# Kernel optimization log

Hardware: AMD Instinct MI355X
Metric: run time of the kernel (lower is better)

Reference implementation:

```python
import jax, jax.numpy as jnp
import numpy as np

B, S, D, H, E, K, F = 8, 2048, 1024, 16, 32, 8, 1024
HD = D // H
EPS = 1e-5


def _ln(x, scale, bias):
    m = jnp.mean(x, axis=-1, keepdims=True)
    v = jnp.mean(jnp.square(x - m), axis=-1, keepdims=True)
    return (x - m) * jax.lax.rsqrt(v + EPS) * scale + bias


def setup_inputs() -> dict:
    key = jax.random.key(0)
    ks = jax.random.split(key, 14)
    w = lambda k, shp: jax.random.normal(k, shp, jnp.float32) * 0.02
    return {
        "hidden_states": jax.random.normal(ks[0], (B, S, D), jnp.float32),
        "ln1_scale": jnp.ones((D,), jnp.float32),
        "ln1_bias": jnp.zeros((D,), jnp.float32),
        "wq": w(ks[1], (D, D)), "bq": jnp.zeros((D,), jnp.float32),
        "wk": w(ks[2], (D, D)), "bk": jnp.zeros((D,), jnp.float32),
        "wv": w(ks[3], (D, D)), "bv": jnp.zeros((D,), jnp.float32),
        "ln2_scale": jnp.ones((D,), jnp.float32),
        "ln2_bias": jnp.zeros((D,), jnp.float32),
        "router_w": w(ks[4], (D, E)), "router_b": jnp.zeros((E,), jnp.float32),
        "w1": w(ks[5], (E, D, F)), "b1": jnp.zeros((E, F), jnp.float32),
        "w2": w(ks[6], (E, F, D)), "b2": jnp.zeros((E, D), jnp.float32),
    }


def reference(hidden_states, ln1_scale, ln1_bias, wq, bq, wk, bk, wv, bv,
              ln2_scale, ln2_bias, router_w, router_b, w1, b1, w2, b2):
    # --- attention sub-block (faithful to source: scores are [B,S,H,H]) ---
    x = _ln(hidden_states, ln1_scale, ln1_bias)
    q = (x @ wq + bq).reshape(B, S, H, HD)
    k = (x @ wk + bk).reshape(B, S, H, HD)
    v = (x @ wv + bv).reshape(B, S, H, HD)
    scores = jnp.einsum('bshd,bsgd->bshg', q, k) / np.sqrt(HD).astype(np.float32)
    probs = jax.nn.softmax(scores, axis=-1)
    ctx = jnp.einsum('bshg,bsgd->bshd', probs, v).reshape(B, S, D)
    h1 = hidden_states + ctx
    # --- MoE sub-block: per-token top-K of E experts ---
    x2 = _ln(h1, ln2_scale, ln2_bias)
    router_probs = jax.nn.softmax(x2 @ router_w + router_b, axis=-1)  # [B,S,E]
    top_w, top_i = jax.lax.top_k(router_probs, K)
    top_w = top_w / jnp.sum(top_w, axis=-1, keepdims=True)
    # dense per-token gate over experts (zero for unselected)
    gates = jnp.sum(jax.nn.one_hot(top_i, E, dtype=x2.dtype) * top_w[..., None], axis=-2)  # [B,S,E]
    moe = jnp.zeros_like(x2)
    for e in range(E):  # fixed small expert set; unrolled under jit
        h = jax.nn.gelu(x2 @ w1[e] + b1[e], approximate=False)
        moe = moe + gates[..., e:e + 1] * (h @ w2[e] + b2[e])
    return h1 + moe
```

## Files before the change

kernel.cpp:

```cpp
#include <hip/hip_runtime.h>
#include <hip/hip_bf16.h>
#include <stdint.h>

#define TOK 16384
#define DD  1024
#define NE  32

typedef unsigned short u16;
typedef __attribute__((ext_vector_type(8))) short short8;
typedef __attribute__((ext_vector_type(4))) float f32x4;

__device__ __forceinline__ u16 f2bf(float f) {
  unsigned int u = __float_as_uint(f);
  u += 0x7fffu + ((u >> 16) & 1u);
  return (u16)(u >> 16);
}
__device__ __forceinline__ float bf2f(u16 h) {
  return __uint_as_float(((unsigned int)h) << 16);
}
__device__ __forceinline__ void gload16(const void* g, void* l) {
  __builtin_amdgcn_global_load_lds((const __attribute__((address_space(1))) void*)g,
                                   (__attribute__((address_space(3))) void*)l, 16, 0, 0);
}

__global__ __launch_bounds__(256) void k_transpose(const float* __restrict__ src,
                                                   u16* __restrict__ dst, int R, int C) {
  __shared__ float tile[32][33];
  size_t mb = (size_t)blockIdx.z * R * C;
  int c0 = blockIdx.x * 32, r0 = blockIdx.y * 32;
  int tx = threadIdx.x, ty = threadIdx.y;
#pragma unroll
  for (int i = 0; i < 4; i++)
    tile[ty + i * 8][tx] = src[mb + (size_t)(r0 + ty + i * 8) * C + c0 + tx];
  __syncthreads();
#pragma unroll
  for (int i = 0; i < 4; i++) {
    float v = tile[tx][ty + i * 8];
    dst[mb + (size_t)(c0 + ty + i * 8) * R + r0 + tx] = f2bf(v);
  }
}

__global__ __launch_bounds__(256) void k_transpose_split(const float* __restrict__ src,
                                                         u16* __restrict__ hi,
                                                         u16* __restrict__ lo, int R, int C) {
  __shared__ float tile[32][33];
  int c0 = blockIdx.x * 32, r0 = blockIdx.y * 32;
  int tx = threadIdx.x, ty = threadIdx.y;
#pragma unroll
  for (int i = 0; i < 4; i++)
    tile[ty + i * 8][tx] = src[(size_t)(r0 + ty + i * 8) * C + c0 + tx];
  __syncthreads();
#pragma unroll
  for (int i = 0; i < 4; i++) {
    float v = tile[tx][ty + i * 8];
    u16 h = f2bf(v);
    u16 l = f2bf(v - bf2f(h));
    size_t idx = (size_t)(c0 + ty + i * 8) * R + r0 + tx;
    hi[idx] = h;
    lo[idx] = l;
  }
}

__global__ __launch_bounds__(256) void k_ln1(const float* __restrict__ x,
                                             const float* __restrict__ sc,
                                             const float* __restrict__ bi,
                                             u16* __restrict__ ohi, u16* __restrict__ olo) {
  __shared__ float red[10];
  int t = blockIdx.x, tid = threadIdx.x;
  size_t base = (size_t)t * DD + tid * 4;
  float4 v = *(const float4*)(x + base);
  float s1 = v.x + v.y + v.z + v.w;
  float s2 = v.x * v.x + v.y * v.y + v.z * v.z + v.w * v.w;
  for (int o = 1; o < 64; o <<= 1) { s1 += __shfl_xor(s1, o, 64); s2 += __shfl_xor(s2, o, 64); }
  int wid = tid >> 6;
  if ((tid & 63) == 0) { red[wid * 2] = s1; red[wid * 2 + 1] = s2; }
  __syncthreads();
  if (tid == 0) {
    float a = 0, b = 0;
    for (int i = 0; i < 4; i++) { a += red[i * 2]; b += red[i * 2 + 1]; }
    float mean = a * (1.f / DD);
    float var = b * (1.f / DD) - mean * mean;
    red[8] = mean; red[9] = rsqrtf(var + 1e-5f);
  }
  __syncthreads();
  float mean = red[8], rs = red[9];
  int e0 = tid * 4;
  float xv[4] = {v.x, v.y, v.z, v.w};
  ushort4 oh, ol;
  u16* ph = (u16*)&oh; u16* pl = (u16*)&ol;
#pragma unroll
  for (int i = 0; i < 4; i++) {
    float f = (xv[i] - mean) * rs * sc[e0 + i] + bi[e0 + i];
    u16 h = f2bf(f);
    ph[i] = h;
    pl[i] = f2bf(f - bf2f(h));
  }
  *(ushort4*)(ohi + base) = oh;
  *(ushort4*)(olo + base) = ol;
}

__global__ __launch_bounds__(256) void k_attn(
    const float* __restrict__ hidden, const float* __restrict__ qb,
    const float* __restrict__ kb, const float* __restrict__ vb,
    const float* __restrict__ ln2s, const float* __restrict__ ln2b,
    const float* __restrict__ rw, const float* __restrict__ rb,
    float* __restrict__ out, u16* __restrict__ x2b, float* __restrict__ gates) {
  __shared__ float qs[16][68], ks[16][68], vs[16][68];
  __shared__ float probs[16][17];
  __shared__ float x2s[1024];
  __shared__ float red[12];
  __shared__ float part[8][32];
  int t = blockIdx.x, tid = threadIdx.x;
  size_t base = (size_t)t * DD + tid * 4;
  int hh = tid >> 4, dd = (tid & 15) * 4;
  {
    float4 q4 = *(const float4*)(qb + base);
    float4 k4 = *(const float4*)(kb + base);
    float4 v4 = *(const float4*)(vb + base);
    qs[hh][dd + 0] = q4.x; qs[hh][dd + 1] = q4.y; qs[hh][dd + 2] = q4.z; qs[hh][dd + 3] = q4.w;
    ks[hh][dd + 0] = k4.x; ks[hh][dd + 1] = k4.y; ks[hh][dd + 2] = k4.z; ks[hh][dd + 3] = k4.w;
    vs[hh][dd + 0] = v4.x; vs[hh][dd + 1] = v4.y; vs[hh][dd + 2] = v4.z; vs[hh][dd + 3] = v4.w;
  }
  __syncthreads();
  {
    int g = tid & 15;
    float s = 0.f;
#pragma unroll
    for (int d = 0; d < 64; d++) s += qs[hh][d] * ks[g][d];
    s *= 0.125f;
    float mx = s;
    for (int o = 1; o < 16; o <<= 1) mx = fmaxf(mx, __shfl_xor(mx, o, 16));
    float p = __expf(s - mx);
    float sm = p;
    for (int o = 1; o < 16; o <<= 1) sm += __shfl_xor(sm, o, 16);
    probs[hh][g] = p / sm;
  }
  __syncthreads();
  float c0 = 0, c1 = 0, c2 = 0, c3 = 0;
#pragma unroll
  for (int g = 0; g < 16; g++) {
    float pw = probs[hh][g];
    c0 += pw * vs[g][dd + 0]; c1 += pw * vs[g][dd + 1];
    c2 += pw * vs[g][dd + 2]; c3 += pw * vs[g][dd + 3];
  }
  float4 hv = *(const float4*)(hidden + base);
  float h0 = hv.x + c0, h1 = hv.y + c1, h2 = hv.z + c2, h3 = hv.w + c3;
  { float4 o4; o4.x = h0; o4.y = h1; o4.z = h2; o4.w = h3; *(float4*)(out + base) = o4; }
  float s1 = h0 + h1 + h2 + h3;
  float s2 = h0 * h0 + h1 * h1 + h2 * h2 + h3 * h3;
  for (int o = 1; o < 64; o <<= 1) { s1 += __shfl_xor(s1, o, 64); s2 += __shfl_xor(s2, o, 64); }
  int wid = tid >> 6;
  if ((tid & 63) == 0) { red[wid * 2] = s1; red[wid * 2 + 1] = s2; }
  __syncthreads();
  if (tid == 0) {
    float a = 0, b = 0;
    for (int i = 0; i < 4; i++) { a += red[i * 2]; b += red[i * 2 + 1]; }
    float mean = a * (1.f / DD);
    float var = b * (1.f / DD) - mean * mean;
    red[8] = mean; red[9] = rsqrtf(var + 1e-5f);
  }
  __syncthreads();
  float mean = red[8], rs = red[9];
  int e0 = tid * 4;
  float x0 = (h0 - mean) * rs * ln2s[e0 + 0] + ln2b[e0 + 0];
  float x1 = (h1 - mean) * rs * ln2s[e0 + 1] + ln2b[e0 + 1];
  float x2 = (h2 - mean) * rs * ln2s[e0 + 2] + ln2b[e0 + 2];
  float x3 = (h3 - mean) * rs * ln2s[e0 + 3] + ln2b[e0 + 3];
  ushort4 xo; xo.x = f2bf(x0); xo.y = f2bf(x1); xo.z = f2bf(x2); xo.w = f2bf(x3);
  *(ushort4*)(x2b + base) = xo;
  x2s[e0 + 0] = x0; x2s[e0 + 1] = x1; x2s[e0 + 2] = x2; x2s[e0 + 3] = x3;
  __syncthreads();
  {
    int e = tid & 31, seg = tid >> 5;
    const float* rwp = rw + (size_t)(seg * 128) * NE + e;
    float acc = 0.f;
#pragma unroll 8
    for (int i = 0; i < 128; i++) acc += x2s[seg * 128 + i] * rwp[(size_t)i * NE];
    part[seg][e] = acc;
  }
  __syncthreads();
  if (tid < 32) {
    float l = rb[tid];
#pragma unroll
    for (int s = 0; s < 8; s++) l += part[s][tid];
    float mx = l;
    for (int o = 1; o < 32; o <<= 1) mx = fmaxf(mx, __shfl_xor(mx, o, 32));
    float p = __expf(l - mx);
    float sm = p;
    for (int o = 1; o < 32; o <<= 1) sm += __shfl_xor(sm, o, 32);
    p /= sm;
    bool sel = false;
#pragma unroll
    for (int rsel = 0; rsel < 8; rsel++) {
      float bv = sel ? -1.f : p;
      int bi_ = tid;
      for (int o = 1; o < 32; o <<= 1) {
        float ov = __shfl_xor(bv, o, 32);
        int oi = __shfl_xor(bi_, o, 32);
        if (ov > bv || (ov == bv && oi < bi_)) { bv = ov; bi_ = oi; }
      }
      if (tid == bi_) sel = true;
    }
    float wsel = sel ? p : 0.f;
    float ts = wsel;
    for (int o = 1; o < 32; o <<= 1) ts += __shfl_xor(ts, o, 32);
    gates[(size_t)t * 32 + tid] = sel ? (p / ts) : 0.f;
  }
}

__global__ void k_zero32(int* p) { int i = threadIdx.x; if (i < 32) p[i] = 0; }

__global__ void k_listbuild(const float* __restrict__ gates, int* __restrict__ counts,
                            int* __restrict__ lists, int* __restrict__ slots,
                            float* __restrict__ gsel) {
  int t = blockIdx.x * 256 + threadIdx.x;
  int j = 0;
  for (int e = 0; e < NE; e++) {
    float g = gates[(size_t)t * 32 + e];
    if (g > 0.f && j < 8) {
      int pos = atomicAdd(&counts[e], 1);
      lists[(size_t)e * TOK + pos] = t;
      slots[t * 8 + j] = (e << 14) | pos;
      gsel[t * 8 + j] = g;
      j++;
    }
  }
}

__global__ void k_scan(const int* __restrict__ counts, int* __restrict__ segoff) {
  if (threadIdx.x == 0) { int s = 0; for (int e = 0; e < NE; e++) { segoff[e] = s; s += counts[e]; } }
}

__global__ __launch_bounds__(256) void k_gemm_p(
    const u16* __restrict__ Ahi, const u16* __restrict__ Alo,
    const u16* __restrict__ qkvT,
    const float* __restrict__ bq, const float* __restrict__ bk, const float* __restrict__ bv,
    float* __restrict__ Cbase) {
  constexpr int KD = 1024;
  __shared__ alignas(16) u16 As[2][2][128 * 32];
  __shared__ alignas(16) u16 Bs[2][2][128 * 32];
  const int tid = threadIdx.x;
  const int w = tid >> 6, lane = tid & 63;
  const int bm = blockIdx.x, bn = blockIdx.y, z = blockIdx.z;
  const u16* Bhi = qkvT + (size_t)z * (2u * KD * KD);
  const u16* Blo = Bhi + (size_t)KD * KD;
  const float* bias = (z == 0) ? bq : (z == 1) ? bk : bv;
  float* C = Cbase + (size_t)z * TOK * KD;

  int rowA[2], qA[2], rowB[2];
#pragma unroll
  for (int i = 0; i < 2; i++) {
    int c = (w * 2 + i) * 64 + lane;
    int r = c >> 2;
    qA[i] = c & 3;
    rowB[i] = bn * 128 + r;
    rowA[i] = bm * 128 + r;
  }

  auto stage = [&](int buf, int k0) {
#pragma unroll
    for (int i = 0; i < 2; i++) {
      size_t ga = (size_t)rowA[i] * KD + k0 + qA[i] * 8;
      size_t gb = (size_t)rowB[i] * KD + k0 + qA[i] * 8;
      int lo_off = (w * 2 + i) * 1024;
      gload16(Ahi + ga, (char*)&As[buf][0][0] + lo_off);
      gload16(Alo + ga, (char*)&As[buf][1][0] + lo_off);
      gload16(Bhi + gb, (char*)&Bs[buf][0][0] + lo_off);
      gload16(Blo + gb, (char*)&Bs[buf][1][0] + lo_off);
    }
  };

  f32x4 acc[4][4];
#pragma unroll
  for (int m = 0; m < 4; m++)
#pragma unroll
    for (int n = 0; n < 4; n++) acc[m][n] = (f32x4)0.f;

  const int wr = (w >> 1) * 64, wc = (w & 1) * 64;
  const int la = lane & 15, lk = (lane >> 4) * 8;

  stage(0, 0);
  __syncthreads();
  for (int kt = 0; kt < 32; kt++) {
    const int cur = kt & 1;
    if (kt + 1 < 32) stage(cur ^ 1, (kt + 1) * 32);
    short8 ah[4], al[4], bh[4], bl[4];
#pragma unroll
    for (int m = 0; m < 4; m++) {
      ah[m] = *(const short8*)&As[cur][0][(wr + m * 16 + la) * 32 + lk];
      al[m] = *(const short8*)&As[cur][1][(wr + m * 16 + la) * 32 + lk];
    }
#pragma unroll
    for (int n = 0; n < 4; n++) {
      bh[n] = *(const short8*)&Bs[cur][0][(wc + n * 16 + la) * 32 + lk];
      bl[n] = *(const short8*)&Bs[cur][1][(wc + n * 16 + la) * 32 + lk];
    }
#pragma unroll
    for (int m = 0; m < 4; m++)
#pragma unroll
      for (int n = 0; n < 4; n++) {
        acc[m][n] = __builtin_amdgcn_mfma_f32_16x16x32_bf16(ah[m], bh[n], acc[m][n], 0, 0, 0);
        acc[m][n] = __builtin_amdgcn_mfma_f32_16x16x32_bf16(ah[m], bl[n], acc[m][n], 0, 0, 0);
        acc[m][n] = __builtin_amdgcn_mfma_f32_16x16x32_bf16(al[m], bh[n], acc[m][n], 0, 0, 0);
      }
    __syncthreads();
  }

  const int rl4 = (lane >> 4) * 4;
#pragma unroll
  for (int m = 0; m < 4; m++) {
#pragma unroll
    for (int n = 0; n < 4; n++) {
      const int col = bn * 128 + wc + n * 16 + la;
      const float bvv = bias[col];
      f32x4 a4 = acc[m][n];
#pragma unroll
      for (int r = 0; r < 4; r++) {
        const int grow = bm * 128 + wr + m * 16 + rl4 + r;
        C[(size_t)grow * KD + col] = a4[r] + bvv;
      }
    }
  }
}

__global__ __launch_bounds__(256) void k_gemm1(
    const u16* __restrict__ A, const u16* __restrict__ BT, const float* __restrict__ bias,
    u16* __restrict__ Cb, const int* __restrict__ lists, const int* __restrict__ counts,
    const int* __restrict__ segoff) {
  constexpr int KD = 1024;
  __shared__ alignas(16) u16 As[2][128 * 32];
  __shared__ alignas(16) u16 Bs[2][128 * 32];

  int e = (int)blockIdx.z;
  int count = counts[e];
  if ((int)blockIdx.x * 128 >= count) return;
  const int* list = lists + (size_t)e * TOK;
  int so = segoff[e];
  const u16* Bp = BT + (size_t)e * (KD * KD);
  const float* bp = bias + (size_t)e * KD;

  const int tid = threadIdx.x;
  const int w = tid >> 6, lane = tid & 63;
  const int bm = blockIdx.x, bn = blockIdx.y;

  int rowA[2], qA[2], rowB[2];
#pragma unroll
  for (int i = 0; i < 2; i++) {
    int c = (w * 2 + i) * 64 + lane;
    int r = c >> 2;
    qA[i] = c & 3;
    rowB[i] = bn * 128 + r;
    int rr = bm * 128 + r;
    rowA[i] = (rr < count) ? list[rr] : 0;
  }

  auto stage = [&](int buf, int k0) {
#pragma unroll
    for (int i = 0; i < 2; i++) {
      gload16(A + (size_t)rowA[i] * KD + k0 + qA[i] * 8,
              (char*)&As[buf][0] + (w * 2 + i) * 1024);
      gload16(Bp + (size_t)rowB[i] * KD + k0 + qA[i] * 8,
              (char*)&Bs[buf][0] + (w * 2 + i) * 1024);
    }
  };

  f32x4 acc[4][4];
#pragma unroll
  for (int m = 0; m < 4; m++)
#pragma unroll
    for (int n = 0; n < 4; n++) acc[m][n] = (f32x4)0.f;

  const int wr = (w >> 1) * 64, wc = (w & 1) * 64;
  const int la = lane & 15, lk = (lane >> 4) * 8;

  stage(0, 0);
  __syncthreads();
#pragma unroll 2
  for (int kt = 0; kt < 32; kt++) {
    const int cur = kt & 1;
    if (kt + 1 < 32) stage(cur ^ 1, (kt + 1) * 32);
    short8 af[4], bf8[4];
#pragma unroll
    for (int m = 0; m < 4; m++)
      af[m] = *(const short8*)&As[cur][(wr + m * 16 + la) * 32 + lk];
#pragma unroll
    for (int n = 0; n < 4; n++)
      bf8[n] = *(const short8*)&Bs[cur][(wc + n * 16 + la) * 32 + lk];
#pragma unroll
    for (int m = 0; m < 4; m++)
#pragma unroll
      for (int n = 0; n < 4; n++)
        acc[m][n] = __builtin_amdgcn_mfma_f32_16x16x32_bf16(af[m], bf8[n], acc[m][n], 0, 0, 0);
    __syncthreads();
  }

  const int rl4 = (lane >> 4) * 4;
#pragma unroll
  for (int m = 0; m < 4; m++) {
#pragma unroll
    for (int n = 0; n < 4; n++) {
      const int col = bn * 128 + wc + n * 16 + la;
      const float bvv = bp[col];
      f32x4 a4 = acc[m][n];
#pragma unroll
      for (int r = 0; r < 4; r++) {
        const int grow = bm * 128 + wr + m * 16 + rl4 + r;
        if (grow < count) {
          float v = a4[r] + bvv;
          float gx = 0.5f * v * (1.0f + erff(v * 0.70710678f));
          Cb[(size_t)(so + grow) * KD + col] = f2bf(gx);
        }
      }
    }
  }
}

__global__ __launch_bounds__(256) void k_gemm2(
    const u16* __restrict__ A, const u16* __restrict__ BT, const float* __restrict__ bias,
    u16* __restrict__ out2, const int* __restrict__ counts, const int* __restrict__ segoff,
    int col0, int C) {
  constexpr int KD = 1024;
  __shared__ alignas(16) u16 As[2][128 * 32];
  __shared__ alignas(16) u16 Bs[2][128 * 32];

  int e = (int)blockIdx.z;
  int count = counts[e];
  if ((int)blockIdx.x * 128 >= count) return;
  int so = segoff[e];
  const u16* Bp = BT + (size_t)e * (KD * KD);
  const float* bp = bias + (size_t)e * KD;

  const int tid = threadIdx.x;
  const int w = tid >> 6, lane = tid & 63;
  const int bm = blockIdx.x, bn = blockIdx.y;

  int rowA[2], qA[2], rowB[2];
#pragma unroll
  for (int i = 0; i < 2; i++) {
    int c = (w * 2 + i) * 64 + lane;
    int r = c >> 2;
    qA[i] = c & 3;
    rowB[i] = col0 + bn * 128 + r;
    int rr = bm * 128 + r;
    rowA[i] = so + ((rr < count) ? rr : 0);
  }

  auto stage = [&](int buf, int k0) {
#pragma unroll
    for (int i = 0; i < 2; i++) {
      gload16(A + (size_t)rowA[i] * KD + k0 + qA[i] * 8,
              (char*)&As[buf][0] + (w * 2 + i) * 1024);
      gload16(Bp + (size_t)rowB[i] * KD + k0 + qA[i] * 8,
              (char*)&Bs[buf][0] + (w * 2 + i) * 1024);
    }
  };

  f32x4 acc[4][4];
#pragma unroll
  for (int m = 0; m < 4; m++)
#pragma unroll
    for (int n = 0; n < 4; n++) acc[m][n] = (f32x4)0.f;

  const int wr = (w >> 1) * 64, wc = (w & 1) * 64;
  const int la = lane & 15, lk = (lane >> 4) * 8;

  stage(0, 0);
  __syncthreads();
#pragma unroll 2
  for (int kt = 0; kt < 32; kt++) {
    const int cur = kt & 1;
    if (kt + 1 < 32) stage(cur ^ 1, (kt + 1) * 32);
    short8 af[4], bf8[4];
#pragma unroll
    for (int m = 0; m < 4; m++)
      af[m] = *(const short8*)&As[cur][(wr + m * 16 + la) * 32 + lk];
#pragma unroll
    for (int n = 0; n < 4; n++)
      bf8[n] = *(const short8*)&Bs[cur][(wc + n * 16 + la) * 32 + lk];
#pragma unroll
    for (int m = 0; m < 4; m++)
#pragma unroll
      for (int n = 0; n < 4; n++)
        acc[m][n] = __builtin_amdgcn_mfma_f32_16x16x32_bf16(af[m], bf8[n], acc[m][n], 0, 0, 0);
    __syncthreads();
  }

  const int rl4 = (lane >> 4) * 4;
#pragma unroll
  for (int m = 0; m < 4; m++) {
#pragma unroll
    for (int n = 0; n < 4; n++) {
      const int lcol = bn * 128 + wc + n * 16 + la;
      const float bvv = bp[col0 + lcol];
      f32x4 a4 = acc[m][n];
#pragma unroll
      for (int r = 0; r < 4; r++) {
        const int grow = bm * 128 + wr + m * 16 + rl4 + r;
        if (grow < count)
          out2[(size_t)(so + grow) * C + lcol] = f2bf(a4[r] + bvv);
      }
    }
  }
}

__global__ __launch_bounds__(256) void k_gather(
    const float* __restrict__ gsel, const int* __restrict__ slots,
    const int* __restrict__ segoff, const u16* __restrict__ out2,
    float* __restrict__ out, int col0, int C, int cshift) {
  int tid4 = threadIdx.x * 4;
  int tpb = 1024 >> cshift;
  int t = blockIdx.x * tpb + (tid4 >> cshift);
  int c4 = tid4 & (C - 1);
  float a0 = 0, a1 = 0, a2 = 0, a3 = 0;
#pragma unroll
  for (int j = 0; j < 8; j++) {
    int s = slots[t * 8 + j];
    float g = gsel[t * 8 + j];
    int seg = segoff[s >> 14] + (s & 16383);
    ushort4 v4 = *(const ushort4*)(out2 + (size_t)seg * C + c4);
    a0 += g * bf2f(v4.x); a1 += g * bf2f(v4.y);
    a2 += g * bf2f(v4.z); a3 += g * bf2f(v4.w);
  }
  size_t ob = (size_t)t * DD + col0 + c4;
  float4 o = *(const float4*)(out + ob);
  o.x += a0; o.y += a1; o.z += a2; o.w += a3;
  *(float4*)(out + ob) = o;
}

extern "C" void kernel_launch(void* const* d_in, const int* in_sizes, int n_in,
                              void* d_out, int out_size, void* d_ws, size_t ws_size,
                              hipStream_t stream) {
  (void)in_sizes; (void)n_in; (void)out_size;
  const float* hidden = (const float*)d_in[0];
  const float* ln1s = (const float*)d_in[1];
  const float* ln1b = (const float*)d_in[2];
  const float* wq = (const float*)d_in[3];
  const float* bq = (const float*)d_in[4];
  const float* wk = (const float*)d_in[5];
  const float* bk = (const float*)d_in[6];
  const float* wv = (const float*)d_in[7];
  const float* bv = (const float*)d_in[8];
  const float* ln2s = (const float*)d_in[9];
  const float* ln2b = (const float*)d_in[10];
  const float* rw = (const float*)d_in[11];
  const float* rb = (const float*)d_in[12];
  const float* w1 = (const float*)d_in[13];
  const float* b1 = (const float*)d_in[14];
  const float* w2 = (const float*)d_in[15];
  const float* b2 = (const float*)d_in[16];
  float* out = (float*)d_out;

  char* wsp = (char*)d_ws;
  size_t off = 0;
  auto alloc = [&](size_t b) -> void* {
    void* p = wsp + off;
    off += (b + 255) & ~(size_t)255;
    return p;
  };
  u16* wT = (u16*)alloc((size_t)NE * DD * DD * 2);
  int* slots = (int*)alloc((size_t)TOK * 8 * 4);
  float* gsel = (float*)alloc((size_t)TOK * 8 * 4);
  int* counts = (int*)alloc(NE * 4);
  int* segoff = (int*)alloc((NE + 1) * 4);
  u16* x_hi = (u16*)alloc((size_t)TOK * DD * 2);
  float* gates = (float*)alloc((size_t)TOK * NE * 4);
  int* lists = (int*)alloc((size_t)NE * TOK * 4);
  char* pool = (char*)alloc((size_t)TOK * 8 * DD * 2);
  u16* qkvT = (u16*)pool;
  u16* x_lo = (u16*)(pool + 12u * 1024 * 1024);
  float* qkv = (float*)(pool + 44u * 1024 * 1024);
  float* qbuf = qkv;
  float* kbuf = qkv + (size_t)TOK * DD;
  float* vbuf = qkv + 2 * (size_t)TOK * DD;
  u16* h_buf = (u16*)pool;

  const size_t ROWS = (size_t)TOK * 8;
  size_t extra = (ws_size > off) ? ws_size - off : 0;
  int C;
  u16* out2;
  if (extra >= ROWS * 1024 * 2 + 1024) { C = 1024; out2 = (u16*)alloc(ROWS * 1024 * 2); }
  else if (extra >= ROWS * 512 * 2 + 1024) { C = 512; out2 = (u16*)alloc(ROWS * 512 * 2); }
  else if (extra >= ROWS * 256 * 2 + 1024) { C = 256; out2 = (u16*)alloc(ROWS * 256 * 2); }
  else { C = 128; out2 = (u16*)x_hi; }
  int cshift = 31 - __builtin_clz((unsigned)C);

  dim3 tb32(32, 8, 1);
  k_zero32<<<1, 64, 0, stream>>>(counts);
  k_transpose_split<<<dim3(32, 32, 1), tb32, 0, stream>>>(wq, qkvT, qkvT + (size_t)DD * DD, DD, DD);
  k_transpose_split<<<dim3(32, 32, 1), tb32, 0, stream>>>(wk, qkvT + 2 * (size_t)DD * DD, qkvT + 3 * (size_t)DD * DD, DD, DD);
  k_transpose_split<<<dim3(32, 32, 1), tb32, 0, stream>>>(wv, qkvT + 4 * (size_t)DD * DD, qkvT + 5 * (size_t)DD * DD, DD, DD);
  k_transpose<<<dim3(32, 32, NE), tb32, 0, stream>>>(w1, wT, DD, DD);
  k_ln1<<<TOK, 256, 0, stream>>>(hidden, ln1s, ln1b, x_hi, x_lo);
  k_gemm_p<<<dim3(128, 8, 3), 256, 0, stream>>>(x_hi, x_lo, qkvT, bq, bk, bv, qkv);
  k_attn<<<TOK, 256, 0, stream>>>(hidden, qbuf, kbuf, vbuf, ln2s, ln2b, rw, rb, out, x_hi, gates);
  k_listbuild<<<TOK / 256, 256, 0, stream>>>(gates, counts, lists, slots, gsel);
  k_scan<<<1, 32, 0, stream>>>(counts, segoff);
  k_gemm1<<<dim3(128, 8, NE), 256, 0, stream>>>(x_hi, wT, b1, h_buf, lists, counts, segoff);
  k_transpose<<<dim3(32, 32, NE), tb32, 0, stream>>>(w2, wT, DD, DD);
  for (int c0 = 0; c0 < DD; c0 += C) {
    k_gemm2<<<dim3(128, C / 128, NE), 256, 0, stream>>>(h_buf, wT, b2, out2, counts, segoff, c0, C);
    k_gather<<<TOK >> (10 - cshift), 256, 0, stream>>>(gsel, slots, segoff, out2, out, c0, C, cshift);
  }
}
```

Measured before the change: 2.037 ms.

## Move router to MFMA kernel, swizzle LDS in GEMMs, use polynomial GELU

The router projection moves out of the per-token attention kernel into a separate MFMA GEMM that uses split hi/lo bf16 inputs. Top-k selection and list building are fused into one warp-per-token kernel that uses ballot/popc. All three GEMMs now XOR-swizzle their LDS layout to reduce bank conflicts. The exact erf GELU is replaced by an Abramowitz-Stegun polynomial. This adds a kernel launch and a logits buffer, and the approximate GELU and split-bf16 router may shift numerics and expert selection slightly.

```diff
diff --git a/kernel.cpp b/kernel.cpp
--- a/kernel.cpp
+++ b/kernel.cpp
@@ -21,6 +21,16 @@
 __device__ __forceinline__ void gload16(const void* g, void* l) {
   __builtin_amdgcn_global_load_lds((const __attribute__((address_space(1))) void*)g,
                                    (__attribute__((address_space(3))) void*)l, 16, 0, 0);
+}
+__device__ __forceinline__ float fast_gelu(float v) {
+  float s = v * 0.70710678118f;
+  float a = fabsf(s);
+  float t = 1.0f / fmaf(0.3275911f, a, 1.0f);
+  float poly = t * fmaf(t, fmaf(t, fmaf(t, fmaf(t, 1.061405429f, -1.453152027f),
+                                        1.421413741f), -0.284496736f), 0.254829592f);
+  float er = 1.0f - poly * __expf(-s * s);
+  er = copysignf(er, s);
+  return 0.5f * v * (1.0f + er);
 }
 
 __global__ __launch_bounds__(256) void k_transpose(const float* __restrict__ src,
@@ -103,13 +113,10 @@
     const float* __restrict__ hidden, const float* __restrict__ qb,
     const float* __restrict__ kb, const float* __restrict__ vb,
     const float* __restrict__ ln2s, const float* __restrict__ ln2b,
-    const float* __restrict__ rw, const float* __restrict__ rb,
-    float* __restrict__ out, u16* __restrict__ x2b, float* __restrict__ gates) {
+    float* __restrict__ out, u16* __restrict__ x2hi, u16* __restrict__ x2lo) {
   __shared__ float qs[16][68], ks[16][68], vs[16][68];
   __shared__ float probs[16][17];
-  __shared__ float x2s[1024];
   __shared__ float red[12];
-  __shared__ float part[8][32];
   int t = blockIdx.x, tid = threadIdx.x;
   size_t base = (size_t)t * DD + tid * 4;
   int hh = tid >> 4, dd = (tid & 15) * 4;
@@ -162,68 +169,106 @@
   __syncthreads();
   float mean = red[8], rs = red[9];
   int e0 = tid * 4;
-  float x0 = (h0 - mean) * rs * ln2s[e0 + 0] + ln2b[e0 + 0];
-  float x1 = (h1 - mean) * rs * ln2s[e0 + 1] + ln2b[e0 + 1];
-  float x2 = (h2 - mean) * rs * ln2s[e0 + 2] + ln2b[e0 + 2];
-  float x3 = (h3 - mean) * rs * ln2s[e0 + 3] + ln2b[e0 + 3];
-  ushort4 xo; xo.x = f2bf(x0); xo.y = f2bf(x1); xo.z = f2bf(x2); xo.w = f2bf(x3);
-  *(ushort4*)(x2b + base) = xo;
-  x2s[e0 + 0] = x0; x2s[e0 + 1] = x1; x2s[e0 + 2] = x2; x2s[e0 + 3] = x3;
-  __syncthreads();
-  {
-    int e = tid & 31, seg = tid >> 5;
-    const float* rwp = rw + (size_t)(seg * 128) * NE + e;
-    float acc = 0.f;
-#pragma unroll 8
-    for (int i = 0; i < 128; i++) acc += x2s[seg * 128 + i] * rwp[(size_t)i * NE];
-    part[seg][e] = acc;
-  }
-  __syncthreads();
-  if (tid < 32) {
-    float l = rb[tid];
-#pragma unroll
-    for (int s = 0; s < 8; s++) l += part[s][tid];
-    float mx = l;
-    for (int o = 1; o < 32; o <<= 1) mx = fmaxf(mx, __shfl_xor(mx, o, 32));
-    float p = __expf(l - mx);
-    float sm = p;
-    for (int o = 1; o < 32; o <<= 1) sm += __shfl_xor(sm, o, 32);
-    p /= sm;
-    bool sel = false;
-#pragma unroll
-    for (int rsel = 0; rsel < 8; rsel++) {
-      float bv = sel ? -1.f : p;
-      int bi_ = tid;
-      for (int o = 1; o < 32; o <<= 1) {
-        float ov = __shfl_xor(bv, o, 32);
-        int oi = __shfl_xor(bi_, o, 32);
-        if (ov > bv || (ov == bv && oi < bi_)) { bv = ov; bi_ = oi; }
-      }
-      if (tid == bi_) sel = true;
-    }
-    float wsel = sel ? p : 0.f;
-    float ts = wsel;
-    for (int o = 1; o < 32; o <<= 1) ts += __shfl_xor(ts, o, 32);
-    gates[(size_t)t * 32 + tid] = sel ? (p / ts) : 0.f;
+  float hvv[4] = {h0, h1, h2, h3};
+  ushort4 oh, ol;
+  u16* ph = (u16*)&oh; u16* pl = (u16*)&ol;
+#pragma unroll
+  for (int i = 0; i < 4; i++) {
+    float f = (hvv[i] - mean) * rs * ln2s[e0 + i] + ln2b[e0 + i];
+    u16 h = f2bf(f);
+    ph[i] = h;
+    pl[i] = f2bf(f - bf2f(h));
+  }
+  *(ushort4*)(x2hi + base) = oh;
+  *(ushort4*)(x2lo + base) = ol;
+}
+
+__global__ __launch_bounds__(256) void k_router(
+    const u16* __restrict__ Xhi, const u16* __restrict__ Xlo,
+    const u16* __restrict__ Bh_, const u16* __restrict__ Bl_,
+    const float* __restrict__ rb, float* __restrict__ logits) {
+  __shared__ alignas(16) u16 Ah[64 * 32], Al[64 * 32], Bh[32 * 32], Bl[32 * 32];
+  int tid = threadIdx.x;
+  int w = tid >> 6, lane = tid & 63;
+  int t0 = (int)blockIdx.x * 64;
+  int row = tid >> 2, q = tid & 3;
+  int cb = tid & 127, rowb = cb >> 2, qb2 = cb & 3;
+  f32x4 acc[2];
+  acc[0] = (f32x4)0.f; acc[1] = (f32x4)0.f;
+  const int la = lane & 15, lk = (lane >> 4) * 8;
+  const int m0 = w * 16;
+  for (int kt = 0; kt < 32; kt++) {
+    int k0 = kt * 32;
+    __syncthreads();
+    gload16(Xhi + (size_t)(t0 + row) * DD + k0 + q * 8, (char*)Ah + tid * 16);
+    gload16(Xlo + (size_t)(t0 + row) * DD + k0 + q * 8, (char*)Al + tid * 16);
+    if (tid < 128)
+      gload16(Bh_ + (size_t)rowb * DD + k0 + qb2 * 8, (char*)Bh + cb * 16);
+    else
+      gload16(Bl_ + (size_t)rowb * DD + k0 + qb2 * 8, (char*)Bl + cb * 16);
+    __syncthreads();
+    short8 ah = *(const short8*)&Ah[(m0 + la) * 32 + lk];
+    short8 al = *(const short8*)&Al[(m0 + la) * 32 + lk];
+#pragma unroll
+    for (int n = 0; n < 2; n++) {
+      short8 bh = *(const short8*)&Bh[(n * 16 + la) * 32 + lk];
+      short8 bl = *(const short8*)&Bl[(n * 16 + la) * 32 + lk];
+      acc[n] = __builtin_amdgcn_mfma_f32_16x16x32_bf16(ah, bh, acc[n], 0, 0, 0);
+      acc[n] = __builtin_amdgcn_mfma_f32_16x16x32_bf16(ah, bl, acc[n], 0, 0, 0);
+      acc[n] = __builtin_amdgcn_mfma_f32_16x16x32_bf16(al, bh, acc[n], 0, 0, 0);
+    }
+  }
+  int rl4 = (lane >> 4) * 4;
+#pragma unroll
+  for (int n = 0; n < 2; n++) {
+    int col = n * 16 + la;
+    float bias = rb[col];
+#pragma unroll
+    for (int r = 0; r < 4; r++) {
+      int grow = t0 + m0 + rl4 + r;
+      logits[(size_t)grow * NE + col] = acc[n][r] + bias;
+    }
   }
 }
 
 __global__ void k_zero32(int* p) { int i = threadIdx.x; if (i < 32) p[i] = 0; }
 
-__global__ void k_listbuild(const float* __restrict__ gates, int* __restrict__ counts,
-                            int* __restrict__ lists, int* __restrict__ slots,
-                            float* __restrict__ gsel) {
-  int t = blockIdx.x * 256 + threadIdx.x;
-  int j = 0;
-  for (int e = 0; e < NE; e++) {
-    float g = gates[(size_t)t * 32 + e];
-    if (g > 0.f && j < 8) {
-      int pos = atomicAdd(&counts[e], 1);
-      lists[(size_t)e * TOK + pos] = t;
-      slots[t * 8 + j] = (e << 14) | pos;
-      gsel[t * 8 + j] = g;
-      j++;
-    }
+__global__ __launch_bounds__(256) void k_topk(
+    const float* __restrict__ logits, int* __restrict__ counts,
+    int* __restrict__ lists, int* __restrict__ slots, float* __restrict__ gsel) {
+  int tid = threadIdx.x;
+  int t = blockIdx.x * 8 + (tid >> 5);
+  int e = tid & 31;
+  int sub = (tid >> 5) & 1;
+  float l = logits[(size_t)t * NE + e];
+  float mx = l;
+  for (int o = 1; o < 32; o <<= 1) mx = fmaxf(mx, __shfl_xor(mx, o, 32));
+  float p = __expf(l - mx);
+  float sm = p;
+  for (int o = 1; o < 32; o <<= 1) sm += __shfl_xor(sm, o, 32);
+  p /= sm;
+  bool sel = false;
+#pragma unroll
+  for (int r = 0; r < 8; r++) {
+    float bv = sel ? -1.f : p;
+    int bi_ = e;
+    for (int o = 1; o < 32; o <<= 1) {
+      float ov = __shfl_xor(bv, o, 32);
+      int oi = __shfl_xor(bi_, o, 32);
+      if (ov > bv || (ov == bv && oi < bi_)) { bv = ov; bi_ = oi; }
+    }
+    if (e == bi_) sel = true;
+  }
+  float ts = sel ? p : 0.f;
+  for (int o = 1; o < 32; o <<= 1) ts += __shfl_xor(ts, o, 32);
+  unsigned long long bm = __ballot(sel);
+  unsigned m32 = (unsigned)(bm >> (sub * 32));
+  if (sel) {
+    int j = __popc(m32 & ((1u << e) - 1u));
+    int pos = atomicAdd(&counts[e], 1);
+    lists[(size_t)e * TOK + pos] = t;
+    slots[t * 8 + j] = (e << 14) | pos;
+    gsel[t * 8 + j] = p / ts;
   }
 }
 
@@ -252,7 +297,7 @@
   for (int i = 0; i < 2; i++) {
     int c = (w * 2 + i) * 64 + lane;
     int r = c >> 2;
-    qA[i] = c & 3;
+    qA[i] = (c & 3) ^ ((c >> 3) & 3);
     rowB[i] = bn * 128 + r;
     rowA[i] = bm * 128 + r;
   }
@@ -277,7 +322,9 @@
     for (int n = 0; n < 4; n++) acc[m][n] = (f32x4)0.f;
 
   const int wr = (w >> 1) * 64, wc = (w & 1) * 64;
-  const int la = lane & 15, lk = (lane >> 4) * 8;
+  const int la = lane & 15;
+  const int sA = (((lane >> 4) ^ (((wr + la) >> 1) & 3)) * 8);
+  const int sB = (((lane >> 4) ^ (((wc + la) >> 1) & 3)) * 8);
 
   stage(0, 0);
   __syncthreads();
@@ -287,13 +334,13 @@
     short8 ah[4], al[4], bh[4], bl[4];
 #pragma unroll
     for (int m = 0; m < 4; m++) {
-      ah[m] = *(const short8*)&As[cur][0][(wr + m * 16 + la) * 32 + lk];
-      al[m] = *(const short8*)&As[cur][1][(wr + m * 16 + la) * 32 + lk];
+      ah[m] = *(const short8*)&As[cur][0][(wr + m * 16 + la) * 32 + sA];
+      al[m] = *(const short8*)&As[cur][1][(wr + m * 16 + la) * 32 + sA];
     }
 #pragma unroll
     for (int n = 0; n < 4; n++) {
-      bh[n] = *(const short8*)&Bs[cur][0][(wc + n * 16 + la) * 32 + lk];
-      bl[n] = *(const short8*)&Bs[cur][1][(wc + n * 16 + la) * 32 + lk];
+      bh[n] = *(const short8*)&Bs[cur][0][(wc + n * 16 + la) * 32 + sB];
+      bl[n] = *(const short8*)&Bs[cur][1][(wc + n * 16 + la) * 32 + sB];
     }
 #pragma unroll
     for (int m = 0; m < 4; m++)
@@ -348,7 +395,7 @@
   for (int i = 0; i < 2; i++) {
     int c = (w * 2 + i) * 64 + lane;
     int r = c >> 2;
-    qA[i] = c & 3;
+    qA[i] = (c & 3) ^ ((c >> 3) & 3);
     rowB[i] = bn * 128 + r;
     int rr = bm * 128 + r;
     rowA[i] = (rr < count) ? list[rr] : 0;
@@ -371,7 +418,9 @@
     for (int n = 0; n < 4; n++) acc[m][n] = (f32x4)0.f;
 
   const int wr = (w >> 1) * 64, wc = (w & 1) * 64;
-  const int la = lane & 15, lk = (lane >> 4) * 8;
+  const int la = lane & 15;
+  const int sA = (((lane >> 4) ^ (((wr + la) >> 1) & 3)) * 8);
+  const int sB = (((lane >> 4) ^ (((wc + la) >> 1) & 3)) * 8);
 
   stage(0, 0);
   __syncthreads();
@@ -382,10 +431,10 @@
     short8 af[4], bf8[4];
 #pragma unroll
     for (int m = 0; m < 4; m++)
-      af[m] = *(const short8*)&As[cur][(wr + m * 16 + la) * 32 + lk];
+      af[m] = *(const short8*)&As[cur][(wr + m * 16 + la) * 32 + sA];
 #pragma unroll
     for (int n = 0; n < 4; n++)
-      bf8[n] = *(const short8*)&Bs[cur][(wc + n * 16 + la) * 32 + lk];
+      bf8[n] = *(const short8*)&Bs[cur][(wc + n * 16 + la) * 32 + sB];
 #pragma unroll
     for (int m = 0; m < 4; m++)
 #pragma unroll
@@ -405,11 +454,8 @@
 #pragma unroll
       for (int r = 0; r < 4; r++) {
         const int grow = bm * 128 + wr + m * 16 + rl4 + r;
-        if (grow < count) {
-          float v = a4[r] + bvv;
-          float gx = 0.5f * v * (1.0f + erff(v * 0.70710678f));
-          Cb[(size_t)(so + grow) * KD + col] = f2bf(gx);
-        }
+        if (grow < count)
+          Cb[(size_t)(so + grow) * KD + col] = f2bf(fast_gelu(a4[r] + bvv));
       }
     }
   }
@@ -439,7 +485,7 @@
   for (int i = 0; i < 2; i++) {
     int c = (w * 2 + i) * 64 + lane;
     int r = c >> 2;
-    qA[i] = c & 3;
+    qA[i] = (c & 3) ^ ((c >> 3) & 3);
     rowB[i] = col0 + bn * 128 + r;
     int rr = bm * 128 + r;
     rowA[i] = so + ((rr < count) ? rr : 0);
@@ -462,7 +508,9 @@
     for (int n = 0; n < 4; n++) acc[m][n] = (f32x4)0.f;
 
   const int wr = (w >> 1) * 64, wc = (w & 1) * 64;
-  const int la = lane & 15, lk = (lane >> 4) * 8;
+  const int la = lane & 15;
+  const int sA = (((lane >> 4) ^ (((wr + la) >> 1) & 3)) * 8);
+  const int sB = (((lane >> 4) ^ (((wc + la) >> 1) & 3)) * 8);
 
   stage(0, 0);
   __syncthreads();
@@ -473,10 +521,10 @@
     short8 af[4], bf8[4];
 #pragma unroll
     for (int m = 0; m < 4; m++)
-      af[m] = *(const short8*)&As[cur][(wr + m * 16 + la) * 32 + lk];
+      af[m] = *(const short8*)&As[cur][(wr + m * 16 + la) * 32 + sA];
 #pragma unroll
     for (int n = 0; n < 4; n++)
-      bf8[n] = *(const short8*)&Bs[cur][(wc + n * 16 + la) * 32 + lk];
+      bf8[n] = *(const short8*)&Bs[cur][(wc + n * 16 + la) * 32 + sB];
 #pragma unroll
     for (int m = 0; m < 4; m++)
 #pragma unroll
@@ -562,8 +610,10 @@
   float* gsel = (float*)alloc((size_t)TOK * 8 * 4);
   int* counts = (int*)alloc(NE * 4);
   int* segoff = (int*)alloc((NE + 1) * 4);
+  u16* rwTh = (u16*)alloc((size_t)NE * DD * 2);
+  u16* rwTl = (u16*)alloc((size_t)NE * DD * 2);
+  float* logits = (float*)alloc((size_t)TOK * NE * 4);
   u16* x_hi = (u16*)alloc((size_t)TOK * DD * 2);
-  float* gates = (float*)alloc((size_t)TOK * NE * 4);
   int* lists = (int*)alloc((size_t)NE * TOK * 4);
   char* pool = (char*)alloc((size_t)TOK * 8 * DD * 2);
   u16* qkvT = (u16*)pool;
@@ -589,11 +639,13 @@
   k_transpose_split<<<dim3(32, 32, 1), tb32, 0, stream>>>(wq, qkvT, qkvT + (size_t)DD * DD, DD, DD);
   k_transpose_split<<<dim3(32, 32, 1), tb32, 0, stream>>>(wk, qkvT + 2 * (size_t)DD * DD, qkvT + 3 * (size_t)DD * DD, DD, DD);
   k_transpose_split<<<dim3(32, 32, 1), tb32, 0, stream>>>(wv, qkvT + 4 * (size_t)DD * DD, qkvT + 5 * (size_t)DD * DD, DD, DD);
+  k_transpose_split<<<dim3(1, 32, 1), tb32, 0, stream>>>(rw, rwTh, rwTl, DD, NE);
   k_transpose<<<dim3(32, 32, NE), tb32, 0, stream>>>(w1, wT, DD, DD);
   k_ln1<<<TOK, 256, 0, stream>>>(hidden, ln1s, ln1b, x_hi, x_lo);
   k_gemm_p<<<dim3(128, 8, 3), 256, 0, stream>>>(x_hi, x_lo, qkvT, bq, bk, bv, qkv);
-  k_attn<<<TOK, 256, 0, stream>>>(hidden, qbuf, kbuf, vbuf, ln2s, ln2b, rw, rb, out, x_hi, gates);
-  k_listbuild<<<TOK / 256, 256, 0, stream>>>(gates, counts, lists, slots, gsel);
+  k_attn<<<TOK, 256, 0, stream>>>(hidden, qbuf, kbuf, vbuf, ln2s, ln2b, out, x_hi, x_lo);
+  k_router<<<TOK / 64, 256, 0, stream>>>(x_hi, x_lo, rwTh, rwTl, rb, logits);
+  k_topk<<<TOK / 8, 256, 0, stream>>>(logits, counts, lists, slots, gsel);
   k_scan<<<1, 32, 0, stream>>>(counts, segoff);
   k_gemm1<<<dim3(128, 8, NE), 256, 0, stream>>>(x_hi, wT, b1, h_buf, lists, counts, segoff);
   k_transpose<<<dim3(32, 32, NE), tb32, 0, stream>>>(w2, wT, DD, DD);
```

After: 2.061 ms. No clear change (+1.2%).
